# Optimization experiments

Hardware: AMD Instinct MI355X
Metric: run time of the kernel (lower is better)

## Reference

```python
import jax, jax.numpy as jnp
import numpy as np

NEG_INF = -1e30
NA_POS = 3  # position of the 'no-answer' token (after [CLS], yes, no)


def mask_pos0(x, mask):
    # keep x where mask==1, set to large negative where mask==0
    return x * mask + (1.0 - mask) * NEG_INF


def make_span_mask(seq_len, max_ans_len):
    m = jnp.tril(jnp.triu(jnp.ones((seq_len, seq_len), jnp.float32), 0), max_ans_len - 1)
    m = m.at[:4, :].set(0.0)
    m = m.at[1, 1].set(1.0)
    m = m.at[2, 2].set(1.0)
    m = m.at[NA_POS, NA_POS].set(1.0)
    return m


def setup_inputs() -> dict:
    key = jax.random.key(0)
    k1, k2, k3 = jax.random.split(key, 3)
    B, S, H = 8, 4096, 1024
    seq_hiddens = jax.random.normal(k1, (B, S, H), jnp.float32)
    ans_mask = jnp.ones((B, S), jnp.float32)
    W_qa = jax.random.normal(k2, (H, 2), jnp.float32) * (1.0 / np.sqrt(H))
    b_qa = jnp.zeros((2,), jnp.float32)
    return {"seq_hiddens": seq_hiddens, "ans_mask": ans_mask, "W_qa": W_qa,
            "b_qa": b_qa, "top_k": 5}


def reference(seq_hiddens, ans_mask, W_qa, b_qa, top_k):
    B, S, H = seq_hiddens.shape
    max_ans_len = 30
    # linear QA head: (B,S,H) @ (H,2) -> (B,S,2)
    span_logits = jnp.einsum('bsh,hc->bsc', seq_hiddens, W_qa) + b_qa
    masked_span_logits = mask_pos0(span_logits, ans_mask[:, :, None])
    start_logits = masked_span_logits[..., 0]  # (B,S)
    end_logits = masked_span_logits[..., 1]    # (B,S)
    # outer-sum span scores: (B,S,S)
    span_scores = start_logits[:, :, None] + end_logits[:, None, :]
    span_mask = make_span_mask(S, max_ans_len)[None]
    masked_span_scores = mask_pos0(span_scores, span_mask)
    flat = masked_span_scores.reshape(B, S * S)
    _, top_span = jax.lax.top_k(flat, top_k)  # (B,k)
    top_start = top_span // S
    top_end = top_span % S
    return start_logits, end_logits, top_start, top_end
```

## Files before the change

kernel.cpp:

```cpp
#include <hip/hip_runtime.h>
#include <cfloat>

#define NEG_INF_F (-1e30f)

constexpr int BB = 8, SS = 4096, HH = 1024;
constexpr int TOTAL = BB * SS;
constexpr int MAXLEN = 30;
constexpr int RPB = 256;
constexpr int BLK_PER_B = SS / RPB;
constexpr int S1_GRID = BB * BLK_PER_B;

__global__ __launch_bounds__(256) void qa_logits_kernel(
    const float* __restrict__ X,
    const float* __restrict__ mask,
    const float* __restrict__ W,
    const float* __restrict__ bqa,
    float* __restrict__ out) {
  int row  = (int)((blockIdx.x * (size_t)blockDim.x + threadIdx.x) >> 6);
  int lane = threadIdx.x & 63;
  if (row >= TOTAL) return;
  const float* rp = X + (size_t)row * HH;
  float s0 = 0.f, s1 = 0.f;
#pragma unroll
  for (int k = 0; k < HH / 256; ++k) {
    int h = (k * 64 + lane) * 4;
    const float4 x   = *reinterpret_cast<const float4*>(rp + h);
    const float4 w01 = *reinterpret_cast<const float4*>(W + 2 * h);
    const float4 w23 = *reinterpret_cast<const float4*>(W + 2 * h + 4);
    s0 += x.x * w01.x + x.y * w01.z + x.z * w23.x + x.w * w23.z;
    s1 += x.x * w01.y + x.y * w01.w + x.z * w23.y + x.w * w23.w;
  }
#pragma unroll
  for (int off = 32; off > 0; off >>= 1) {
    s0 += __shfl_down(s0, off);
    s1 += __shfl_down(s1, off);
  }
  if (lane == 0) {
    float m = mask[row];
    float inv = 1.f - m;
    out[row]         = (s0 + bqa[0]) * m + inv * NEG_INF_F;
    out[TOTAL + row] = (s1 + bqa[1]) * m + inv * NEG_INF_F;
  }
}

__device__ __forceinline__ unsigned long long pack_key(float v, unsigned idx) {
  unsigned u = __float_as_uint(v);
  u = (u & 0x80000000u) ? ~u : (u | 0x80000000u);
  return ((unsigned long long)u << 32) | (unsigned long long)(0xFFFFFFFFu - idx);
}

__device__ __forceinline__ void k5_insert(unsigned long long k[5], unsigned long long nk) {
  if (nk <= k[4]) return;
  k[4] = nk;
  unsigned long long t;
  if (k[4] > k[3]) { t = k[3]; k[3] = k[4]; k[4] = t; }
  if (k[3] > k[2]) { t = k[2]; k[2] = k[3]; k[3] = t; }
  if (k[2] > k[1]) { t = k[1]; k[1] = k[2]; k[2] = t; }
  if (k[1] > k[0]) { t = k[0]; k[0] = k[1]; k[1] = t; }
}

__device__ __forceinline__ void wave_top5_u64(unsigned long long k[5],
                                              unsigned long long r[5]) {
#pragma unroll
  for (int q = 0; q < 5; ++q) {
    unsigned long long m = k[0];
    if (k[1] > m) m = k[1];
    if (k[2] > m) m = k[2];
    if (k[3] > m) m = k[3];
    if (k[4] > m) m = k[4];
#pragma unroll
    for (int off = 1; off < 64; off <<= 1) {
      unsigned long long o = __shfl_xor(m, off);
      if (o > m) m = o;
    }
    r[q] = m;
#pragma unroll
    for (int p = 0; p < 5; ++p)
      if (k[p] == m) k[p] = 0ull;
  }
}

__global__ __launch_bounds__(RPB) void topk_stage1(
    const float* __restrict__ logits,
    unsigned long long* __restrict__ ws) {
  const int b  = blockIdx.x / BLK_PER_B;
  const int rb = blockIdx.x % BLK_PER_B;
  const int i0 = rb * RPB;
  const int t  = (int)threadIdx.x;
  const int lane = t & 63;
  const int w = t >> 6;

  __shared__ float s_st[RPB];
  __shared__ float s_en[RPB + 32];
  __shared__ unsigned long long sk[(RPB / 64) * 5];

  const float* st = logits + (size_t)b * SS + i0;
  const float* en = logits + (size_t)(BB + b) * SS + i0;
  const int n_en = min(SS - i0, RPB + MAXLEN - 1);

  if (t < RPB / 4)
    *reinterpret_cast<float4*>(&s_st[t * 4]) =
        *reinterpret_cast<const float4*>(st + t * 4);
  else if (t >= 64 && t < 64 + (n_en + 3) / 4) {
    int r = t - 64;
    if (r * 4 + 4 <= n_en)
      *reinterpret_cast<float4*>(&s_en[r * 4]) =
          *reinterpret_cast<const float4*>(en + r * 4);
    else
      for (int c = r * 4; c < n_en; ++c) s_en[c] = en[c];
  }
  __syncthreads();

  unsigned long long k5[5] = {0, 0, 0, 0, 0};
  const int i = i0 + t;
  if (i >= 4) {
    float sv = s_st[t];
    unsigned base = (unsigned)(i * SS + i);
    int cap = n_en - t;
#pragma unroll
    for (int c = 0; c < MAXLEN; ++c)
      if (c < cap) k5_insert(k5, pack_key(sv + s_en[t + c], base + c));
  } else if (i >= 1) {
    k5_insert(k5, pack_key(s_st[t] + s_en[t], (unsigned)(i * SS + i)));
  }

  unsigned long long r5[5];
  wave_top5_u64(k5, r5);
  if (lane == 0) {
#pragma unroll
    for (int q = 0; q < 5; ++q) sk[w * 5 + q] = r5[q];
  }
  __syncthreads();

  if (w == 0) {
    unsigned long long m5[5] = {0, 0, 0, 0, 0};
    if (lane < (RPB / 64) * 5) m5[0] = sk[lane];
    unsigned long long f5[5];
    wave_top5_u64(m5, f5);
    if (lane == 0) {
#pragma unroll
      for (int q = 0; q < 5; ++q) ws[blockIdx.x * 5 + q] = f5[q];
    }
  }
}

__global__ __launch_bounds__(64) void topk_stage2(
    const unsigned long long* __restrict__ ws,
    float* __restrict__ out) {
  const int b = blockIdx.x;
  const int lane = (int)threadIdx.x;
  const unsigned long long* src = ws + (size_t)b * BLK_PER_B * 5;

  unsigned long long k5[5] = {0, 0, 0, 0, 0};
  k5[0] = src[lane];
  if (lane < BLK_PER_B * 5 - 64) k5[1] = src[64 + lane];

  unsigned long long r5[5];
  wave_top5_u64(k5, r5);

  if (lane == 0) {
    float* ts = out + 2 * (size_t)TOTAL;
    float* te = ts + BB * 5;
#pragma unroll
    for (int q = 0; q < 5; ++q) {
      unsigned idx = 0xFFFFFFFFu - (unsigned)(r5[q] & 0xFFFFFFFFull);
      ts[b * 5 + q] = (float)(idx >> 12);
      te[b * 5 + q] = (float)(idx & (SS - 1));
    }
  }
}

extern "C" void kernel_launch(void* const* d_in, const int* in_sizes, int n_in,
                              void* d_out, int out_size, void* d_ws, size_t ws_size,
                              hipStream_t stream) {
  const float* X    = (const float*)d_in[0];
  const float* mask = (const float*)d_in[1];
  const float* W    = (const float*)d_in[2];
  const float* bqa  = (const float*)d_in[3];
  float* out = (float*)d_out;
  unsigned long long* ws = (unsigned long long*)d_ws;

  qa_logits_kernel<<<TOTAL / 4, 256, 0, stream>>>(X, mask, W, bqa, out);
  topk_stage1<<<S1_GRID, RPB, 0, stream>>>(out, ws);
  topk_stage2<<<BB, 64, 0, stream>>>(ws, out);
}
```

Baseline: 36.53 us.

## Split span candidates across four threads per start row in top-k stage

The first top-k stage now gives each start row four threads, each scoring eight end positions, instead of one thread walking all thirty. Blocks cover 64 rows, so there are four times as many blocks, and stage two reads five partial results per lane to match. The aim is to shorten the serial insert chain per thread and spread the top-k work over more of the GPU. Out-of-range end slots are padded with a large negative value rather than skipped. This is safe only because real candidates always outrank the padded ones.

After: 34.72 us. -5.0%, faster.

```diff
diff --git a/kernel.cpp b/kernel.cpp
--- a/kernel.cpp
+++ b/kernel.cpp
@@ -6,7 +6,9 @@
 constexpr int BB = 8, SS = 4096, HH = 1024;
 constexpr int TOTAL = BB * SS;
 constexpr int MAXLEN = 30;
-constexpr int RPB = 256;
+constexpr int RPB = 64;
+constexpr int TPR = 4;
+constexpr int CPT = 8;
 constexpr int BLK_PER_B = SS / RPB;
 constexpr int S1_GRID = BB * BLK_PER_B;
 
@@ -80,7 +82,7 @@
   }
 }
 
-__global__ __launch_bounds__(RPB) void topk_stage1(
+__global__ __launch_bounds__(256) void topk_stage1(
     const float* __restrict__ logits,
     unsigned long long* __restrict__ ws) {
   const int b  = blockIdx.x / BLK_PER_B;
@@ -92,36 +94,44 @@
 
   __shared__ float s_st[RPB];
   __shared__ float s_en[RPB + 32];
-  __shared__ unsigned long long sk[(RPB / 64) * 5];
+  __shared__ unsigned long long sk[4 * 5];
 
   const float* st = logits + (size_t)b * SS + i0;
   const float* en = logits + (size_t)(BB + b) * SS + i0;
   const int n_en = min(SS - i0, RPB + MAXLEN - 1);
 
-  if (t < RPB / 4)
+  if (t < 16) {
     *reinterpret_cast<float4*>(&s_st[t * 4]) =
         *reinterpret_cast<const float4*>(st + t * 4);
-  else if (t >= 64 && t < 64 + (n_en + 3) / 4) {
-    int r = t - 64;
+  } else if (t < 40) {
+    int r = t - 16;
     if (r * 4 + 4 <= n_en)
       *reinterpret_cast<float4*>(&s_en[r * 4]) =
           *reinterpret_cast<const float4*>(en + r * 4);
     else
-      for (int c = r * 4; c < n_en; ++c) s_en[c] = en[c];
+#pragma unroll
+      for (int c = 0; c < 4; ++c)
+        s_en[r * 4 + c] = (r * 4 + c < n_en) ? en[r * 4 + c] : NEG_INF_F;
   }
   __syncthreads();
 
   unsigned long long k5[5] = {0, 0, 0, 0, 0};
-  const int i = i0 + t;
+  const int lr = t >> 2;
+  const int sub = t & 3;
+  const int i = i0 + lr;
+
   if (i >= 4) {
-    float sv = s_st[t];
-    unsigned base = (unsigned)(i * SS + i);
-    int cap = n_en - t;
+    float sv = s_st[lr];
+    int c0 = sub * CPT;
+    float e[CPT];
 #pragma unroll
-    for (int c = 0; c < MAXLEN; ++c)
-      if (c < cap) k5_insert(k5, pack_key(sv + s_en[t + c], base + c));
-  } else if (i >= 1) {
-    k5_insert(k5, pack_key(s_st[t] + s_en[t], (unsigned)(i * SS + i)));
+    for (int c = 0; c < CPT; ++c)
+      e[c] = (c0 + c < MAXLEN) ? s_en[lr + c0 + c] : NEG_INF_F;
+    unsigned base = (unsigned)(i * SS + i + c0);
+#pragma unroll
+    for (int c = 0; c < CPT; ++c) k5_insert(k5, pack_key(sv + e[c], base + c));
+  } else if (i >= 1 && sub == 0) {
+    k5_insert(k5, pack_key(s_st[lr] + s_en[lr], (unsigned)(i * SS + i)));
   }
 
   unsigned long long r5[5];
@@ -134,7 +144,7 @@
 
   if (w == 0) {
     unsigned long long m5[5] = {0, 0, 0, 0, 0};
-    if (lane < (RPB / 64) * 5) m5[0] = sk[lane];
+    if (lane < 20) m5[0] = sk[lane];
     unsigned long long f5[5];
     wave_top5_u64(m5, f5);
     if (lane == 0) {
@@ -151,9 +161,9 @@
   const int lane = (int)threadIdx.x;
   const unsigned long long* src = ws + (size_t)b * BLK_PER_B * 5;
 
-  unsigned long long k5[5] = {0, 0, 0, 0, 0};
-  k5[0] = src[lane];
-  if (lane < BLK_PER_B * 5 - 64) k5[1] = src[64 + lane];
+  unsigned long long k5[5];
+#pragma unroll
+  for (int q = 0; q < 5; ++q) k5[q] = src[q * 64 + lane];
 
   unsigned long long r5[5];
   wave_top5_u64(k5, r5);
@@ -181,6 +191,6 @@
   unsigned long long* ws = (unsigned long long*)d_ws;
 
   qa_logits_kernel<<<TOTAL / 4, 256, 0, stream>>>(X, mask, W, bqa, out);
-  topk_stage1<<<S1_GRID, RPB, 0, stream>>>(out, ws);
+  topk_stage1<<<S1_GRID, 256, 0, stream>>>(out, ws);
   topk_stage2<<<BB, 64, 0, stream>>>(ws, out);
 }
```
